# Performance work log

Hardware: AMD Instinct MI355X
Metric: run time of the kernel (lower is better)

The kernel has to match this reference:

```python
import jax, jax.numpy as jnp
import numpy as np
from jax import lax

HEADS = 16
HEAD_DIM = 64
EPS = 1e-5

def _act_quant(x):
    # per-token int8 absmax quantization (BitNet b1.58)
    scale = 127.0 / jnp.clip(jnp.max(jnp.abs(x), axis=-1, keepdims=True), EPS)
    return jnp.clip(jnp.round(x * scale), -128.0, 127.0) / scale

def _weight_quant(w):
    # ternary weight quantization with mean-absmax scale
    scale = 1.0 / jnp.clip(jnp.mean(jnp.abs(w)), EPS)
    return jnp.clip(jnp.round(w * scale), -1.0, 1.0) / scale

def bitlinear(x, w):
    # straight-through estimator: forward uses quantized, backward sees identity
    xq = x + lax.stop_gradient(_act_quant(x) - x)
    wq = w + lax.stop_gradient(_weight_quant(w) - w)
    return jnp.einsum('bsd,od->bso', xq, wq)

def setup_inputs() -> dict:
    key = jax.random.key(0)
    ks = jax.random.split(key, 5)
    B, S, D = 2, 2048, 1024
    x = jax.random.normal(ks[0], (B, S, D), dtype=jnp.float32)
    # causal mask (B, 1, S, S): 1 = keep, 0 = masked
    mask = jnp.broadcast_to(jnp.tril(jnp.ones((S, S), dtype=jnp.int32))[None, None], (B, 1, S, S))
    scale = 0.02
    Wq = jax.random.normal(ks[1], (D, D), dtype=jnp.float32) * scale
    Wk = jax.random.normal(ks[2], (D, D), dtype=jnp.float32) * scale
    Wv = jax.random.normal(ks[3], (D, D), dtype=jnp.float32) * scale
    Wo = jax.random.normal(ks[4], (D, D), dtype=jnp.float32) * scale
    return {"x": x, "mask": mask, "Wq": Wq, "Wk": Wk, "Wv": Wv, "Wo": Wo}

def reference(x, mask, Wq, Wk, Wv, Wo):
    B, S, D = x.shape
    H, Hd = HEADS, HEAD_DIM
    q = bitlinear(x, Wq).reshape(B, S, H, Hd).transpose(0, 2, 1, 3)  # (B,H,S,Hd)
    k = bitlinear(x, Wk).reshape(B, S, H, Hd).transpose(0, 2, 1, 3)
    v = bitlinear(x, Wv).reshape(B, S, H, Hd).transpose(0, 2, 1, 3)
    attn = jnp.einsum('bhsd,bhtd->bhst', q, k) / jnp.sqrt(jnp.float32(Hd))
    attn = jnp.where(mask == 0, -jnp.inf, attn)
    attn = jax.nn.softmax(attn, axis=-1)
    out = jnp.einsum('bhst,bhtd->bhsd', attn, v)
    out = out.transpose(0, 2, 1, 3).reshape(B, S, D)
    return bitlinear(out, Wo)
```

## Files before the change

### kernel.cpp

```cpp
#include <hip/hip_runtime.h>
#include <hip/hip_bf16.h>
#include <math.h>


typedef float  f32x4  __attribute__((ext_vector_type(4)));
typedef __bf16 bf16x8 __attribute__((ext_vector_type(8)));
typedef __bf16 bf16x4 __attribute__((ext_vector_type(4)));
typedef unsigned int u32x4 __attribute__((ext_vector_type(4)));

#define EPSV 1e-5f

__device__ __forceinline__ f32x4 mfma16(bf16x8 a, bf16x8 b, f32x4 c) {
    return __builtin_amdgcn_mfma_f32_16x16x32_bf16(a, b, c, 0, 0, 0);
}

__device__ __forceinline__ void gload16(const void* g, void* lds) {
    __builtin_amdgcn_global_load_lds((const __attribute__((address_space(1))) unsigned int*)g,
                                     (__attribute__((address_space(3))) unsigned int*)lds, 16, 0, 0);
}

__global__ __launch_bounds__(256) void k_wsum(const float* __restrict__ w0, const float* __restrict__ w1,
                                              const float* __restrict__ w2, const float* __restrict__ w3,
                                              double* __restrict__ wsum) {
    int w = blockIdx.x >> 6, chunk = blockIdx.x & 63, tid = threadIdx.x;
    const float* W = (w == 0) ? w0 : (w == 1) ? w1 : (w == 2) ? w2 : w3;
    const float* base = W + (size_t)chunk * 16384;
    float s = 0.f;
#pragma unroll
    for (int i = 0; i < 16; i++) {
        f32x4 v = *(const f32x4*)(base + i * 1024 + tid * 4);
        s += fabsf(v.x) + fabsf(v.y) + fabsf(v.z) + fabsf(v.w);
    }
#pragma unroll
    for (int off = 1; off < 64; off <<= 1) s += __shfl_xor(s, off);
    __shared__ float red[4];
    if ((tid & 63) == 0) red[tid >> 6] = s;
    __syncthreads();
    if (tid == 0) {
        double t = (double)red[0] + (double)red[1] + (double)red[2] + (double)red[3];
        atomicAdd(&wsum[w], t);
    }
}

__global__ __launch_bounds__(256) void k_wquant(const float* __restrict__ w0, const float* __restrict__ w1,
                                                const float* __restrict__ w2, const float* __restrict__ w3,
                                                const double* __restrict__ wsum,
                                                __bf16* __restrict__ wq, float* __restrict__ wm) {
    int w = blockIdx.y;
    const float* W = (w == 0) ? w0 : (w == 1) ? w1 : (w == 2) ? w2 : w3;
    float mean = (float)(wsum[w] * (1.0 / 1048576.0));
    float ms = fmaxf(mean, EPSV);
    float scale = 1.0f / ms;
    int pos = blockIdx.x * 1024 + threadIdx.x * 4;
    f32x4 v = *(const f32x4*)(W + pos);
    float q0 = fminf(fmaxf(rintf(v.x * scale), -1.f), 1.f);
    float q1 = fminf(fmaxf(rintf(v.y * scale), -1.f), 1.f);
    float q2 = fminf(fmaxf(rintf(v.z * scale), -1.f), 1.f);
    float q3 = fminf(fmaxf(rintf(v.w * scale), -1.f), 1.f);
    unsigned int b0 = __builtin_bit_cast(unsigned short, (__bf16)q0);
    unsigned int b1 = __builtin_bit_cast(unsigned short, (__bf16)q1);
    unsigned int b2 = __builtin_bit_cast(unsigned short, (__bf16)q2);
    unsigned int b3 = __builtin_bit_cast(unsigned short, (__bf16)q3);
    uint2 p; p.x = b0 | (b1 << 16); p.y = b2 | (b3 << 16);
    *(uint2*)(wq + (size_t)w * 1048576 + pos) = p;
    if (blockIdx.x == 0 && threadIdx.x == 0) wm[w] = ms;
}

__global__ __launch_bounds__(256) void k_actq(const float* __restrict__ in, __bf16* __restrict__ outq,
                                              float* __restrict__ rs) {
    int t = blockIdx.x, tid = threadIdx.x;
    const float* row = in + (size_t)t * 1024;
    f32x4 v = *(const f32x4*)(row + tid * 4);
    float am = fmaxf(fmaxf(fabsf(v.x), fabsf(v.y)), fmaxf(fabsf(v.z), fabsf(v.w)));
#pragma unroll
    for (int off = 1; off < 64; off <<= 1) am = fmaxf(am, __shfl_xor(am, off));
    __shared__ float red[4];
    if ((tid & 63) == 0) red[tid >> 6] = am;
    __syncthreads();
    am = fmaxf(fmaxf(red[0], red[1]), fmaxf(red[2], red[3]));
    am = fmaxf(am, EPSV);
    float scale = 127.0f / am;
    float q0 = fminf(fmaxf(rintf(v.x * scale), -128.f), 127.f);
    float q1 = fminf(fmaxf(rintf(v.y * scale), -128.f), 127.f);
    float q2 = fminf(fmaxf(rintf(v.z * scale), -128.f), 127.f);
    float q3 = fminf(fmaxf(rintf(v.w * scale), -128.f), 127.f);
    unsigned int b0 = __builtin_bit_cast(unsigned short, (__bf16)q0);
    unsigned int b1 = __builtin_bit_cast(unsigned short, (__bf16)q1);
    unsigned int b2 = __builtin_bit_cast(unsigned short, (__bf16)q2);
    unsigned int b3 = __builtin_bit_cast(unsigned short, (__bf16)q3);
    uint2 p; p.x = b0 | (b1 << 16); p.y = b2 | (b3 << 16);
    *(uint2*)(outq + (size_t)t * 1024 + tid * 4) = p;
    if (tid == 0) rs[t] = am / 127.0f;
}

template <int MODE>
__global__ __launch_bounds__(256) void k_gemm(const __bf16* __restrict__ X, const __bf16* __restrict__ Wb,
                                              const float* __restrict__ rs, const float* __restrict__ wm,
                                              __bf16* __restrict__ o0, __bf16* __restrict__ o1,
                                              __bf16* __restrict__ o2, float* __restrict__ outf) {
    __shared__ __attribute__((aligned(16))) __bf16 As[2][4096];
    __shared__ __attribute__((aligned(16))) __bf16 Bs[2][4096];
    int tid = threadIdx.x;
    int wave = tid >> 6, lane = tid & 63, g = lane >> 4, l = lane & 15;
    int m0 = blockIdx.x * 128, n0 = blockIdx.y * 128;
    int z = blockIdx.z;
    const __bf16* W = Wb + (size_t)z * 1048576;
    float wmv = wm[z];
    f32x4 acc[4][4] = {};
    int srow0 = wave * 16 + (lane >> 2);
    int scol = (lane & 3) * 8;
    const __bf16* Ag = X + (size_t)(m0 + srow0) * 1024 + scol;
    const __bf16* Bg = W + (size_t)(n0 + srow0) * 1024 + scol;
    int woff = wave * 512;
    int wrow = (wave >> 1) * 64, wcol = (wave & 1) * 64;
    bool vswap = (MODE == 0) && (z == 2);
    gload16(Ag,             &As[0][woff]);
    gload16(Ag + 64 * 1024, &As[0][woff + 2048]);
    gload16(Bg,             &Bs[0][woff]);
    gload16(Bg + 64 * 1024, &Bs[0][woff + 2048]);
    __syncthreads();
    for (int k0 = 0; k0 < 1024; k0 += 32) {
        int cur = (k0 >> 5) & 1;
        if (k0 + 32 < 1024) {
            int nxt = cur ^ 1;
            gload16(Ag + k0 + 32,             &As[nxt][woff]);
            gload16(Ag + 64 * 1024 + k0 + 32, &As[nxt][woff + 2048]);
            gload16(Bg + k0 + 32,             &Bs[nxt][woff]);
            gload16(Bg + 64 * 1024 + k0 + 32, &Bs[nxt][woff + 2048]);
        }
        bf16x8 af[4], bfr[4];
#pragma unroll
        for (int i = 0; i < 4; i++) af[i]  = *(const bf16x8*)&As[cur][(wrow + i * 16 + l) * 32 + 8 * g];
#pragma unroll
        for (int i = 0; i < 4; i++) bfr[i] = *(const bf16x8*)&Bs[cur][(wcol + i * 16 + l) * 32 + 8 * g];
        if (vswap) {
#pragma unroll
            for (int mi = 0; mi < 4; mi++)
#pragma unroll
                for (int ni = 0; ni < 4; ni++)
                    acc[mi][ni] = mfma16(bfr[ni], af[mi], acc[mi][ni]);
        } else {
#pragma unroll
            for (int mi = 0; mi < 4; mi++)
#pragma unroll
                for (int ni = 0; ni < 4; ni++)
                    acc[mi][ni] = mfma16(af[mi], bfr[ni], acc[mi][ni]);
        }
        __syncthreads();
    }
    if (vswap) {
#pragma unroll
        for (int mi = 0; mi < 4; mi++) {
            int m = m0 + wrow + mi * 16 + l;
            float rsm = rs[m] * wmv;
            int b = m >> 11, s2 = m & 2047;
#pragma unroll
            for (int ni = 0; ni < 4; ni++) {
                int nb = n0 + wcol + ni * 16 + 4 * g;
#pragma unroll
                for (int r = 0; r < 4; r++) {
                    int n = nb + r;
                    int h = n >> 6, hd = n & 63;
                    o2[((size_t)(b * 16 + h) * 64 + hd) * 2048 + s2] = (__bf16)(acc[mi][ni][r] * rsm);
                }
            }
        }
        return;
    }
#pragma unroll
    for (int mi = 0; mi < 4; mi++) {
        int mbase = m0 + wrow + mi * 16 + 4 * g;
        f32x4 rv = {rs[mbase], rs[mbase + 1], rs[mbase + 2], rs[mbase + 3]};
#pragma unroll
        for (int ni = 0; ni < 4; ni++) {
            int n = n0 + wcol + ni * 16 + l;
#pragma unroll
            for (int r = 0; r < 4; r++) {
                float v = acc[mi][ni][r] * (rv[r] * wmv);
                if constexpr (MODE == 0) {
                    int m = mbase + r;
                    int b = m >> 11, s2 = m & 2047;
                    int h = n >> 6, hd = n & 63;
                    __bf16* dst = (z == 0) ? o0 : o1;
                    dst[(((size_t)(b * 16 + h)) * 2048 + s2) * 64 + hd] = (__bf16)v;
                } else {
                    outf[(size_t)(mbase + r) * 1024 + n] = v;
                }
            }
        }
    }
}

__global__ __launch_bounds__(512) void k_attn(const __bf16* __restrict__ qg, const __bf16* __restrict__ kb,
                                              const __bf16* __restrict__ vt, float* __restrict__ attn) {
    __shared__ __attribute__((aligned(16))) __bf16 Ks[3][4096];
    __shared__ __attribute__((aligned(16))) __bf16 Vs[3][4096];
    int tid = threadIdx.x, w = tid >> 6, lane = tid & 63, g = lane >> 4, l = lane & 15;
    int bh = blockIdx.y, bq = bh >> 4, h = bh & 15;
    int xt = (blockIdx.x + blockIdx.y) & 15;
    int xs = (blockIdx.y & 16) ? (15 - xt) : xt;
    int q0 = xs * 128;
    size_t bhq = (size_t)bh * 2048 * 64;
    int qlo = q0 + w * 16, qmax = qlo + 15;
    int qrow = qlo + l;
    bf16x8 aq0 = *(const bf16x8*)(qg + bhq + (size_t)qrow * 64 + 8 * g);
    bf16x8 aq1 = *(const bf16x8*)(qg + bhq + (size_t)qrow * 64 + 32 + 8 * g);
    asm volatile("" : "+v"(aq0), "+v"(aq1));
    f32x4 o[4] = {};
    float mreg = -INFINITY, lsum = 0.f;
    int sRow = w * 8 + (lane >> 3);
    int sCol = ((lane & 7) ^ (lane >> 3)) << 3;
    const __bf16* Kg = kb + bhq + (size_t)sRow * 64 + sCol;
    const __bf16* Vg = vt + bhq + (size_t)sRow * 2048 + sCol;
    int nt = 2 * (xs + 1);
    gload16(Kg,        &Ks[0][w * 512]);
    gload16(Vg,        &Vs[0][w * 512]);
    gload16(Kg + 4096, &Ks[1][w * 512]);
    gload16(Vg + 64,   &Vs[1][w * 512]);
    int cur = 0;
    int swk = (l & 7) << 4;
    for (int t = 0; t < nt; ++t) {
        if (t < nt - 1) { asm volatile("s_waitcnt vmcnt(2)"); }
        else            { asm volatile("s_waitcnt vmcnt(0)"); }
        __builtin_amdgcn_s_barrier();
        __builtin_amdgcn_sched_barrier(0);
        int tn = t + 2;
        if (tn < nt) {
            int nbuf = cur + 2; if (nbuf >= 3) nbuf -= 3;
            gload16(Kg + (size_t)tn * 4096, &Ks[nbuf][w * 512]);
            gload16(Vg + tn * 64,           &Vs[nbuf][w * 512]);
        }
        int t0 = t * 64;
        if (t0 <= qmax) {
            const char* Kb = (const char*)&Ks[cur][0];
            const char* Vb = (const char*)&Vs[cur][0];
            f32x4 sv[4];
            __builtin_amdgcn_s_setprio(1);
#pragma unroll
            for (int nb = 0; nb < 4; nb++) {
                const char* kbase = Kb + (nb * 16 + l) * 128;
                bf16x8 bk0 = *(const bf16x8*)(kbase + ((16 * g) ^ swk));
                bf16x8 bk1 = *(const bf16x8*)(kbase + ((64 + 16 * g) ^ swk));
                f32x4 a = {};
                a = mfma16(bk0, aq0, a);
                a = mfma16(bk1, aq1, a);
                sv[nb] = a * 0.125f;
            }
            __builtin_amdgcn_s_setprio(0);
            if (t0 + 63 > qlo) {
#pragma unroll
                for (int nb = 0; nb < 4; nb++)
#pragma unroll
                    for (int r = 0; r < 4; r++) {
                        int key = t0 + nb * 16 + 4 * g + r;
                        if (key > qrow) sv[nb][r] = -INFINITY;
                    }
            }
            float pm0 = fmaxf(fmaxf(sv[0][0], sv[0][1]), fmaxf(sv[0][2], sv[0][3]));
            float pm1 = fmaxf(fmaxf(sv[1][0], sv[1][1]), fmaxf(sv[1][2], sv[1][3]));
            float pm2 = fmaxf(fmaxf(sv[2][0], sv[2][1]), fmaxf(sv[2][2], sv[2][3]));
            float pm3 = fmaxf(fmaxf(sv[3][0], sv[3][1]), fmaxf(sv[3][2], sv[3][3]));
            float pm = fmaxf(fmaxf(pm0, pm1), fmaxf(pm2, pm3));
            pm = fmaxf(pm, __shfl_xor(pm, 16));
            pm = fmaxf(pm, __shfl_xor(pm, 32));
            float mnew = fmaxf(mreg, pm);
            float corr = __expf(mreg - mnew);
            mreg = mnew;
            float psum = 0.f;
#pragma unroll
            for (int nb = 0; nb < 4; nb++)
#pragma unroll
                for (int r = 0; r < 4; r++) {
                    float pe = __expf(sv[nb][r] - mnew);
                    sv[nb][r] = pe;
                    psum += pe;
                }
            psum += __shfl_xor(psum, 16);
            psum += __shfl_xor(psum, 32);
            lsum = lsum * corr + psum;
#pragma unroll
            for (int hb = 0; hb < 4; hb++) o[hb] *= corr;
            bf16x8 pf0, pf1;
#pragma unroll
            for (int j = 0; j < 8; j++) {
                pf0[j] = (__bf16)sv[j >> 2][j & 3];
                pf1[j] = (__bf16)sv[2 + (j >> 2)][j & 3];
            }
            __builtin_amdgcn_s_setprio(1);
#pragma unroll
            for (int hb = 0; hb < 4; hb++) {
                int vrow = hb * 16 + l;
                const char* vb = Vb + vrow * 128;
                int rsw = vrow & 7;
                int ib = 8 * (g & 1);
                int gh = g >> 1;
                bf16x4 v00 = *(const bf16x4*)(vb + 16 * ((gh + 0) ^ rsw) + ib);
                bf16x4 v01 = *(const bf16x4*)(vb + 16 * ((gh + 2) ^ rsw) + ib);
                bf16x8 vf0 = __builtin_shufflevector(v00, v01, 0, 1, 2, 3, 4, 5, 6, 7);
                o[hb] = mfma16(vf0, pf0, o[hb]);
                bf16x4 v10 = *(const bf16x4*)(vb + 16 * ((gh + 4) ^ rsw) + ib);
                bf16x4 v11 = *(const bf16x4*)(vb + 16 * ((gh + 6) ^ rsw) + ib);
                bf16x8 vf1 = __builtin_shufflevector(v10, v11, 0, 1, 2, 3, 4, 5, 6, 7);
                o[hb] = mfma16(vf1, pf1, o[hb]);
            }
            __builtin_amdgcn_s_setprio(0);
        }
        cur = (cur + 1 == 3) ? 0 : cur + 1;
    }
    float inv = 1.0f / lsum;
    float* dst = attn + ((size_t)(bq * 2048 + qlo + l)) * 1024 + h * 64 + 4 * g;
#pragma unroll
    for (int hb = 0; hb < 4; hb++) {
        f32x4 vsto = o[hb] * inv;
        *(f32x4*)(dst + 16 * hb) = vsto;
    }
}

extern "C" void kernel_launch(void* const* d_in, const int* in_sizes, int n_in,
                              void* d_out, int out_size, void* d_ws, size_t ws_size,
                              hipStream_t stream) {
    const float* x  = (const float*)d_in[0];
    const float* Wq = (const float*)d_in[2];
    const float* Wk = (const float*)d_in[3];
    const float* Wv = (const float*)d_in[4];
    const float* Wo = (const float*)d_in[5];
    float* out = (float*)d_out;
    char* ws = (char*)d_ws;

    double* wsumd = (double*)(ws + 0);
    float*  wmv   = (float*)(ws + 256);
    __bf16* wqall = (__bf16*)(ws + 512);
    __bf16* xq    = (__bf16*)(ws + 512 + 8388608);
    float*  rsx   = (float*)(ws + 512 + 16777216);
    float*  rso   = (float*)(ws + 512 + 16777216 + 16384);
    char*   big   = ws + 512 + 16777216 + 32768;
    __bf16* qbuf  = (__bf16*)(big);
    __bf16* kbuf  = (__bf16*)(big + 8388608);
    __bf16* oq    = (__bf16*)(big + 16777216);
    __bf16* vtb   = (__bf16*)(big + 25165824);
    float*  attn  = (float*)(big + 33554432);

    hipMemsetAsync(ws, 0, 512, stream);
    k_wsum<<<dim3(256), 256, 0, stream>>>(Wq, Wk, Wv, Wo, wsumd);
    k_wquant<<<dim3(1024, 4), 256, 0, stream>>>(Wq, Wk, Wv, Wo, wsumd, wqall, wmv);
    k_actq<<<dim3(4096), 256, 0, stream>>>(x, xq, rsx);
    k_gemm<0><<<dim3(32, 8, 3), 256, 0, stream>>>(xq, wqall, rsx, wmv, qbuf, kbuf, vtb, nullptr);
    k_attn<<<dim3(16, 32), 512, 0, stream>>>(qbuf, kbuf, vtb, attn);
    k_actq<<<dim3(4096), 256, 0, stream>>>(attn, oq, rso);
    k_gemm<1><<<dim3(32, 8, 1), 256, 0, stream>>>(oq, wqall + 3 * 1048576, rso, wmv + 3,
                                                  nullptr, nullptr, nullptr, out);
}
```

Before: 242.9 us.

## Triple-buffer GEMM K-loop with XOR-swizzled LDS and single barrier per step

The bf16 GEMM main loop moves from a double-buffered LDS pipeline with two syncthreads per step to a three-stage ring buffer. Loads are issued two tiles ahead, and explicit vmcnt waits plus one s_barrier replace the trailing sync. The LDS column offset is XOR-swizzled on both the global_load_lds write side and the fragment read side to reduce bank conflicts. MFMA blocks are bracketed with s_setprio. This adds 16KB more LDS per block, which may lower occupancy, and relies on hand-counted vmcnt values being correct.

```diff
diff --git a/kernel.cpp b/kernel.cpp
--- a/kernel.cpp
+++ b/kernel.cpp
@@ -98,8 +98,8 @@
                                               const float* __restrict__ rs, const float* __restrict__ wm,
                                               __bf16* __restrict__ o0, __bf16* __restrict__ o1,
                                               __bf16* __restrict__ o2, float* __restrict__ outf) {
-    __shared__ __attribute__((aligned(16))) __bf16 As[2][4096];
-    __shared__ __attribute__((aligned(16))) __bf16 Bs[2][4096];
+    __shared__ __attribute__((aligned(16))) __bf16 As[3][4096];
+    __shared__ __attribute__((aligned(16))) __bf16 Bs[3][4096];
     int tid = threadIdx.x;
     int wave = tid >> 6, lane = tid & 63, g = lane >> 4, l = lane & 15;
     int m0 = blockIdx.x * 128, n0 = blockIdx.y * 128;
@@ -108,31 +108,41 @@
     float wmv = wm[z];
     f32x4 acc[4][4] = {};
     int srow0 = wave * 16 + (lane >> 2);
-    int scol = (lane & 3) * 8;
+    int scol = 8 * ((lane & 3) ^ ((lane >> 3) & 3));
     const __bf16* Ag = X + (size_t)(m0 + srow0) * 1024 + scol;
     const __bf16* Bg = W + (size_t)(n0 + srow0) * 1024 + scol;
     int woff = wave * 512;
     int wrow = (wave >> 1) * 64, wcol = (wave & 1) * 64;
     bool vswap = (MODE == 0) && (z == 2);
-    gload16(Ag,             &As[0][woff]);
-    gload16(Ag + 64 * 1024, &As[0][woff + 2048]);
-    gload16(Bg,             &Bs[0][woff]);
-    gload16(Bg + 64 * 1024, &Bs[0][woff + 2048]);
-    __syncthreads();
-    for (int k0 = 0; k0 < 1024; k0 += 32) {
-        int cur = (k0 >> 5) & 1;
-        if (k0 + 32 < 1024) {
-            int nxt = cur ^ 1;
-            gload16(Ag + k0 + 32,             &As[nxt][woff]);
-            gload16(Ag + 64 * 1024 + k0 + 32, &As[nxt][woff + 2048]);
-            gload16(Bg + k0 + 32,             &Bs[nxt][woff]);
-            gload16(Bg + 64 * 1024 + k0 + 32, &Bs[nxt][woff + 2048]);
+    const int NT = 32;
+#pragma unroll
+    for (int s = 0; s < 2; s++) {
+        gload16(Ag + s * 32,             &As[s][woff]);
+        gload16(Ag + 64 * 1024 + s * 32, &As[s][woff + 2048]);
+        gload16(Bg + s * 32,             &Bs[s][woff]);
+        gload16(Bg + 64 * 1024 + s * 32, &Bs[s][woff + 2048]);
+    }
+    int cur = 0;
+    int sel8 = 8 * (g ^ ((l >> 1) & 3));
+    for (int t = 0; t < NT; ++t) {
+        if (t < NT - 1) { asm volatile("s_waitcnt vmcnt(4)"); }
+        else            { asm volatile("s_waitcnt vmcnt(0)"); }
+        __builtin_amdgcn_s_barrier();
+        __builtin_amdgcn_sched_barrier(0);
+        int tn = t + 2;
+        if (tn < NT) {
+            int nbuf = cur + 2; if (nbuf >= 3) nbuf -= 3;
+            gload16(Ag + tn * 32,             &As[nbuf][woff]);
+            gload16(Ag + 64 * 1024 + tn * 32, &As[nbuf][woff + 2048]);
+            gload16(Bg + tn * 32,             &Bs[nbuf][woff]);
+            gload16(Bg + 64 * 1024 + tn * 32, &Bs[nbuf][woff + 2048]);
         }
         bf16x8 af[4], bfr[4];
 #pragma unroll
-        for (int i = 0; i < 4; i++) af[i]  = *(const bf16x8*)&As[cur][(wrow + i * 16 + l) * 32 + 8 * g];
-#pragma unroll
-        for (int i = 0; i < 4; i++) bfr[i] = *(const bf16x8*)&Bs[cur][(wcol + i * 16 + l) * 32 + 8 * g];
+        for (int i = 0; i < 4; i++) af[i]  = *(const bf16x8*)&As[cur][(wrow + i * 16 + l) * 32 + sel8];
+#pragma unroll
+        for (int i = 0; i < 4; i++) bfr[i] = *(const bf16x8*)&Bs[cur][(wcol + i * 16 + l) * 32 + sel8];
+        __builtin_amdgcn_s_setprio(1);
         if (vswap) {
 #pragma unroll
             for (int mi = 0; mi < 4; mi++)
@@ -146,7 +156,8 @@
                 for (int ni = 0; ni < 4; ni++)
                     acc[mi][ni] = mfma16(af[mi], bfr[ni], acc[mi][ni]);
         }
-        __syncthreads();
+        __builtin_amdgcn_s_setprio(0);
+        cur = (cur + 1 == 3) ? 0 : cur + 1;
     }
     if (vswap) {
 #pragma unroll
```

After: 240.7 us. No clear change (-0.9%).
